# Performance work log

Measured on AMD Instinct MI355X. Metric: run time of the kernel, lower is better.

The kernel has to match this reference:

```python
import jax, jax.numpy as jnp
import numpy as np

HIDDEN_DIM = 128


def setup_inputs() -> dict:
    key = jax.random.key(0)
    ks = jax.random.split(key, 7)
    n_edges, edge_dim, edge_hidden, d = 20000, 16, 128, HIDDEN_DIM
    h_v = jax.random.normal(ks[0], (n_edges, d), dtype=jnp.float32)
    h_w = jax.random.normal(ks[1], (n_edges, d), dtype=jnp.float32)
    edge_features = jax.random.normal(ks[2], (n_edges, edge_dim), dtype=jnp.float32)
    W1 = jax.random.normal(ks[3], (edge_dim, edge_hidden), dtype=jnp.float32) * (1.0 / np.sqrt(edge_dim))
    b1 = jnp.zeros((edge_hidden,), dtype=jnp.float32)
    W2 = jax.random.normal(ks[4], (edge_hidden, d * d), dtype=jnp.float32) * (1.0 / np.sqrt(edge_hidden))
    b2 = jnp.zeros((d * d,), dtype=jnp.float32)
    return {"h_v": h_v, "h_w": h_w, "edge_features": edge_features,
            "W1": W1, "b1": b1, "W2": W2, "b2": b2}


def reference(h_v, h_w, edge_features, W1, b1, W2, b2):
    d = HIDDEN_DIM
    # Edge MLP: edge_dim -> edge_hidden -> d*d
    hidden = jax.nn.relu(edge_features @ W1 + b1)          # (E, edge_hidden)
    A = (hidden @ W2 + b2).reshape(-1, d, d)               # (E, d, d) per-edge matrices
    # Batched matrix-vector product: messages_e = A_e @ h_w_e
    messages = jnp.einsum('eij,ej->ei', A, h_w)            # (E, d)
    return messages
```

## Files before the change

### kernel.cpp

```cpp
#include <hip/hip_runtime.h>

#define E_EDGES 20000
#define D_DIM   128
#define HS      136

#define NBA 136
#define NBH 313
#define NBC 320

#define SLAB_B 21504

typedef _Float16 f16x8 __attribute__((ext_vector_type(8)));
typedef _Float16 f16x2 __attribute__((ext_vector_type(2)));
typedef float    floatx4 __attribute__((ext_vector_type(4)));

union F8 { f16x8 v; f16x2 h2[4]; unsigned int u[4]; };

__device__ __forceinline__ unsigned short f32_to_f16(float f) {
    _Float16 h = (_Float16)f;
    return __builtin_bit_cast(unsigned short, h);
}

__device__ __forceinline__ void gload_lds16(const void* g, void* l) {
    __builtin_amdgcn_global_load_lds(
        (const __attribute__((address_space(1))) unsigned int*)g,
        (__attribute__((address_space(3))) unsigned int*)l, 16, 0, 0);
}

__global__ __launch_bounds__(256) void prep_all(
    const float* __restrict__ W2, const float* __restrict__ b2,
    const float* __restrict__ ef, const float* __restrict__ W1,
    const float* __restrict__ b1, const float* __restrict__ hw,
    uint4* __restrict__ bpf, char* __restrict__ hslab,
    unsigned short* __restrict__ hwb)
{
    __shared__ __align__(16) char pmem[34816];
    const int bx = blockIdx.x;
    const int t  = threadIdx.x;

    if (bx < NBA) {
        const int h = bx;
        if (h < 129) {
            unsigned short* tile = (unsigned short*)pmem;
            const float* src = (h < 128) ? (W2 + (size_t)h * (D_DIM * D_DIM)) : b2;
            #pragma unroll
            for (int r = 0; r < 16; ++r) {
                const float4 v = ((const float4*)src)[r * 256 + t];
                int c   = (r * 256 + t) * 4;
                int col = c >> 7;
                int k   = c & 127;
                unsigned int u0 = f32_to_f16(v.x) | ((unsigned int)f32_to_f16(v.y) << 16);
                unsigned int u1 = f32_to_f16(v.z) | ((unsigned int)f32_to_f16(v.w) << 16);
                *(uint2*)&tile[col * 136 + k] = make_uint2(u0, u1);
            }
            __syncthreads();
            #pragma unroll
            for (int r2 = 0; r2 < 8; ++r2) {
                int cidx = r2 * 256 + t;
                int ll = cidx & 63;
                int nt = (cidx >> 6) & 1;
                int jq = (cidx >> 7) & 3;
                int ch = (cidx >> 9) & 3;
                int col = 32 * ch + 16 * nt + (ll & 15);
                int k0  = 32 * jq + 8 * (ll >> 4);
                bpf[(size_t)h * 2048 + cidx] = *(const uint4*)&tile[col * 136 + k0];
            }
        } else {
            #pragma unroll
            for (int r2 = 0; r2 < 8; ++r2)
                bpf[(size_t)h * 2048 + r2 * 256 + t] = make_uint4(0, 0, 0, 0);
        }
    } else if (bx < NBA + NBH) {
        float* W1s = (float*)pmem;
        float* b1s = (float*)(pmem + 8192);
        float (*efs)[17] = (float(*)[17])(pmem + 8704);
        const int b  = bx - NBA;
        const int e0 = b * 64;
        #pragma unroll
        for (int i = 0; i < 2; ++i)
            *(float4*)&W1s[(i * 256 + t) * 4] = ((const float4*)W1)[i * 256 + t];
        if (t < 32) *(float4*)&b1s[t * 4] = ((const float4*)b1)[t];
        {
            int e  = t >> 2;
            int k4 = (t & 3) * 4;
            int ge = e0 + e;
            float4 v = make_float4(0.f, 0.f, 0.f, 0.f);
            if (ge < E_EDGES) v = *(const float4*)(ef + (size_t)ge * 16 + k4);
            efs[e][k4 + 0] = v.x; efs[e][k4 + 1] = v.y;
            efs[e][k4 + 2] = v.z; efs[e][k4 + 3] = v.w;
        }
        __syncthreads();
        const int e  = t & 63;
        const int hg = t >> 6;
        const int ge = e0 + e;
        const bool valid = ge < E_EDGES;
        const int eg = ge / 80;
        const int re = ge - eg * 80;
        char* slab = hslab + (size_t)eg * SLAB_B + re * 264;
        float efr[16];
        #pragma unroll
        for (int k = 0; k < 16; ++k) efr[k] = efs[e][k];
        #pragma unroll 4
        for (int hi2 = 0; hi2 < 16; ++hi2) {
            const int h0 = hg * 32 + 2 * hi2;
            float2 bb = *(const float2*)&b1s[h0];
            float a0 = bb.x, a1 = bb.y;
            #pragma unroll
            for (int k = 0; k < 16; ++k) {
                float2 wv = *(const float2*)&W1s[k * 128 + h0];
                a0 += efr[k] * wv.x;
                a1 += efr[k] * wv.y;
            }
            unsigned int pk = (unsigned int)f32_to_f16(fmaxf(a0, 0.f))
                            | ((unsigned int)f32_to_f16(fmaxf(a1, 0.f)) << 16);
            if (valid) *(unsigned int*)(slab + h0 * 2) = pk;
        }
        if (hg == 0 && valid) {
            *(unsigned int*)(slab + 128 * 2) = 0x00003C00u;
            *(unsigned int*)(slab + 130 * 2) = 0u;
        }
    } else {
        int i0 = (bx - NBA - NBH) * 256 + t;
        for (int i = i0; i < (E_EDGES * D_DIM) / 4; i += NBC * 256) {
            const float4 v = ((const float4*)hw)[i];
            union { unsigned short u16[4]; uint2 u2; } o;
            o.u16[0] = f32_to_f16(v.x);
            o.u16[1] = f32_to_f16(v.y);
            o.u16[2] = f32_to_f16(v.z);
            o.u16[3] = f32_to_f16(v.w);
            ((uint2*)hwb)[i] = o.u2;
        }
    }
}

__global__ __launch_bounds__(256, 4)
void edge_main(const uint4* __restrict__ bpf, const char* __restrict__ hslab,
               const uint4* __restrict__ hwb, float* __restrict__ out) {
    __shared__ __align__(16) char slab[SLAB_B];
    const int bx  = blockIdx.x;
    const int ch  = (bx & 7) >> 1;
    const int eg  = (bx >> 3) * 2 + (bx & 1);
    const int tid = threadIdx.x;
    const int jq  = tid >> 6;
    const int l   = tid & 63;
    const int l4  = l >> 4;
    const int lm  = l & 15;
    const int e0  = eg * 80;

    {
        const char* src = hslab + (size_t)eg * SLAB_B;
        for (int i = jq; i < 21; i += 4)
            gload_lds16(src + i * 1024 + l * 16, slab + i * 1024);
    }

    F8 hws[5];
    #pragma unroll
    for (int m = 0; m < 5; ++m)
        hws[m].v = ((const F8*)hwb)[(e0 + 16 * m + lm) * 16 + 4 * jq + l4].v;

    floatx4 C[5][2];
    #pragma unroll
    for (int m = 0; m < 5; ++m)
        #pragma unroll
        for (int nt = 0; nt < 2; ++nt)
            C[m][nt] = (floatx4){0.f, 0.f, 0.f, 0.f};

    __syncthreads();

    const f16x8* bpf8 = (const f16x8*)bpf;
    const int cbase = ch * 512 + jq * 128 + l;

    f16x8 B[2][2];
    auto loadB = [&](int h, f16x8 (&Bq)[2]) {
        const f16x8* p = bpf8 + (size_t)h * 2048 + cbase;
        Bq[0] = p[0];
        Bq[1] = p[64];
    };
    auto doH = [&](int h, const uint2 (&hid)[5]) {
        const int hh = h & 3, p = h & 1;
        #pragma unroll
        for (int m = 0; m < 5; ++m) {
            unsigned int s   = (hh < 2) ? hid[m].x : hid[m].y;
            unsigned int sel = (hh & 1) ? 0x03020302u : 0x01000100u;
            f16x2 d = __builtin_bit_cast(f16x2, __builtin_amdgcn_perm(0u, s, sel));
            F8 a;
            #pragma unroll
            for (int i = 0; i < 4; ++i) a.h2[i] = hws[m].h2[i] * d;
            C[m][0] = __builtin_amdgcn_mfma_f32_16x16x32_f16(a.v, B[p][0], C[m][0], 0, 0, 0);
            C[m][1] = __builtin_amdgcn_mfma_f32_16x16x32_f16(a.v, B[p][1], C[m][1], 0, 0, 0);
        }
        loadB(h + 2, B[p]);
    };

    loadB(0, B[0]);
    loadB(1, B[1]);
    for (int q = 0; q < 33; ++q) {
        uint2 hid[5];
        #pragma unroll
        for (int m = 0; m < 5; ++m)
            hid[m] = *(const uint2*)(slab + (16 * m + lm) * 264 + q * 8);
        doH(4 * q + 0, hid);
        doH(4 * q + 1, hid);
        doH(4 * q + 2, hid);
        doH(4 * q + 3, hid);
    }

    float* red = (float*)slab;
    #pragma unroll 1
    for (int src = 1; src < 4; ++src) {
        __syncthreads();
        if (jq == src) {
            #pragma unroll
            for (int m = 0; m < 5; ++m)
                #pragma unroll
                for (int nt = 0; nt < 2; ++nt)
                    #pragma unroll
                    for (int r = 0; r < 4; ++r)
                        red[((m * 2 + nt) * 4 + r) * 64 + l] = C[m][nt][r];
        }
        __syncthreads();
        if (jq == 0) {
            #pragma unroll
            for (int m = 0; m < 5; ++m)
                #pragma unroll
                for (int nt = 0; nt < 2; ++nt)
                    #pragma unroll
                    for (int r = 0; r < 4; ++r)
                        C[m][nt][r] += red[((m * 2 + nt) * 4 + r) * 64 + l];
        }
    }
    if (jq == 0) {
        #pragma unroll
        for (int m = 0; m < 5; ++m)
            #pragma unroll
            for (int nt = 0; nt < 2; ++nt)
                #pragma unroll
                for (int r = 0; r < 4; ++r)
                    out[(size_t)(e0 + 16 * m + 4 * l4 + r) * D_DIM
                        + 32 * ch + 16 * nt + lm] = C[m][nt][r];
    }
}

extern "C" void kernel_launch(void* const* d_in, const int* in_sizes, int n_in,
                              void* d_out, int out_size, void* d_ws, size_t ws_size,
                              hipStream_t stream) {
    const float* h_w = (const float*)d_in[1];
    const float* ef  = (const float*)d_in[2];
    const float* W1  = (const float*)d_in[3];
    const float* b1  = (const float*)d_in[4];
    const float* W2  = (const float*)d_in[5];
    const float* b2  = (const float*)d_in[6];
    float* out = (float*)d_out;

    char* ws = (char*)d_ws;
    uint4*          bpf   = (uint4*)ws;
    char*           hslab = ws + 4456448;
    unsigned short* hwb   = (unsigned short*)(ws + 4456448 + 5376000);

    hipLaunchKernelGGL(prep_all, dim3(NBA + NBH + NBC), dim3(256), 0, stream,
                       W2, b2, ef, W1, b1, h_w, bpf, hslab, hwb);
    hipLaunchKernelGGL(edge_main, dim3(1000), dim3(256), 0, stream,
                       bpf, hslab, (const uint4*)hwb, out);
}
```

Baseline: 163.6 us.

## Fuse edge MLP hidden layer and h_w conversion into main kernel, widen column tile

The first-layer edge MLP is now computed inside the main kernel with a small fp16 MFMA per 80-edge group and written straight to LDS. h_w is converted to fp16 in registers. This removes the hidden slab and fp16 h_w staging buffers and their extra global round trip. Each block now covers 64 output columns instead of 32, so there are 500 blocks instead of 1000. That halves redundant hidden-layer and h_w work per edge group, but it doubles accumulator registers and lowers the occupancy target to 2 blocks per SIMD group.

New measurement: 161.2 us. About the same (-1.5%).

```diff
diff --git a/kernel.cpp b/kernel.cpp
--- a/kernel.cpp
+++ b/kernel.cpp
@@ -2,144 +2,70 @@
 
 #define E_EDGES 20000
 #define D_DIM   128
-#define HS      136
-
-#define NBA 136
-#define NBH 313
-#define NBC 320
-
-#define SLAB_B 21504
+#define NBA     136
+#define SLAB_B  21504
 
 typedef _Float16 f16x8 __attribute__((ext_vector_type(8)));
+typedef _Float16 f16x4 __attribute__((ext_vector_type(4)));
 typedef _Float16 f16x2 __attribute__((ext_vector_type(2)));
 typedef float    floatx4 __attribute__((ext_vector_type(4)));
 
 union F8 { f16x8 v; f16x2 h2[4]; unsigned int u[4]; };
+union F4 { f16x4 v; f16x2 h2[2]; unsigned int u[2]; };
 
 __device__ __forceinline__ unsigned short f32_to_f16(float f) {
     _Float16 h = (_Float16)f;
     return __builtin_bit_cast(unsigned short, h);
 }
 
-__device__ __forceinline__ void gload_lds16(const void* g, void* l) {
-    __builtin_amdgcn_global_load_lds(
-        (const __attribute__((address_space(1))) unsigned int*)g,
-        (__attribute__((address_space(3))) unsigned int*)l, 16, 0, 0);
-}
-
-__global__ __launch_bounds__(256) void prep_all(
+__global__ __launch_bounds__(256) void prep_w2(
     const float* __restrict__ W2, const float* __restrict__ b2,
-    const float* __restrict__ ef, const float* __restrict__ W1,
-    const float* __restrict__ b1, const float* __restrict__ hw,
-    uint4* __restrict__ bpf, char* __restrict__ hslab,
-    unsigned short* __restrict__ hwb)
+    uint4* __restrict__ bpf)
 {
-    __shared__ __align__(16) char pmem[34816];
-    const int bx = blockIdx.x;
-    const int t  = threadIdx.x;
-
-    if (bx < NBA) {
-        const int h = bx;
-        if (h < 129) {
-            unsigned short* tile = (unsigned short*)pmem;
-            const float* src = (h < 128) ? (W2 + (size_t)h * (D_DIM * D_DIM)) : b2;
-            #pragma unroll
-            for (int r = 0; r < 16; ++r) {
-                const float4 v = ((const float4*)src)[r * 256 + t];
-                int c   = (r * 256 + t) * 4;
-                int col = c >> 7;
-                int k   = c & 127;
-                unsigned int u0 = f32_to_f16(v.x) | ((unsigned int)f32_to_f16(v.y) << 16);
-                unsigned int u1 = f32_to_f16(v.z) | ((unsigned int)f32_to_f16(v.w) << 16);
-                *(uint2*)&tile[col * 136 + k] = make_uint2(u0, u1);
-            }
-            __syncthreads();
-            #pragma unroll
-            for (int r2 = 0; r2 < 8; ++r2) {
-                int cidx = r2 * 256 + t;
-                int ll = cidx & 63;
-                int nt = (cidx >> 6) & 1;
-                int jq = (cidx >> 7) & 3;
-                int ch = (cidx >> 9) & 3;
-                int col = 32 * ch + 16 * nt + (ll & 15);
-                int k0  = 32 * jq + 8 * (ll >> 4);
-                bpf[(size_t)h * 2048 + cidx] = *(const uint4*)&tile[col * 136 + k0];
-            }
-        } else {
-            #pragma unroll
-            for (int r2 = 0; r2 < 8; ++r2)
-                bpf[(size_t)h * 2048 + r2 * 256 + t] = make_uint4(0, 0, 0, 0);
-        }
-    } else if (bx < NBA + NBH) {
-        float* W1s = (float*)pmem;
-        float* b1s = (float*)(pmem + 8192);
-        float (*efs)[17] = (float(*)[17])(pmem + 8704);
-        const int b  = bx - NBA;
-        const int e0 = b * 64;
-        #pragma unroll
-        for (int i = 0; i < 2; ++i)
-            *(float4*)&W1s[(i * 256 + t) * 4] = ((const float4*)W1)[i * 256 + t];
-        if (t < 32) *(float4*)&b1s[t * 4] = ((const float4*)b1)[t];
-        {
-            int e  = t >> 2;
-            int k4 = (t & 3) * 4;
-            int ge = e0 + e;
-            float4 v = make_float4(0.f, 0.f, 0.f, 0.f);
-            if (ge < E_EDGES) v = *(const float4*)(ef + (size_t)ge * 16 + k4);
-            efs[e][k4 + 0] = v.x; efs[e][k4 + 1] = v.y;
-            efs[e][k4 + 2] = v.z; efs[e][k4 + 3] = v.w;
+    __shared__ __align__(16) unsigned short tile[17408];
+    const int h = blockIdx.x;
+    const int t = threadIdx.x;
+
+    if (h < 129) {
+        const float* src = (h < 128) ? (W2 + (size_t)h * (D_DIM * D_DIM)) : b2;
+        #pragma unroll
+        for (int r = 0; r < 16; ++r) {
+            const float4 v = ((const float4*)src)[r * 256 + t];
+            int c   = (r * 256 + t) * 4;
+            int col = c >> 7;
+            int k   = c & 127;
+            unsigned int u0 = f32_to_f16(v.x) | ((unsigned int)f32_to_f16(v.y) << 16);
+            unsigned int u1 = f32_to_f16(v.z) | ((unsigned int)f32_to_f16(v.w) << 16);
+            *(uint2*)&tile[col * 136 + k] = make_uint2(u0, u1);
         }
         __syncthreads();
-        const int e  = t & 63;
-        const int hg = t >> 6;
-        const int ge = e0 + e;
-        const bool valid = ge < E_EDGES;
-        const int eg = ge / 80;
-        const int re = ge - eg * 80;
-        char* slab = hslab + (size_t)eg * SLAB_B + re * 264;
-        float efr[16];
-        #pragma unroll
-        for (int k = 0; k < 16; ++k) efr[k] = efs[e][k];
-        #pragma unroll 4
-        for (int hi2 = 0; hi2 < 16; ++hi2) {
-            const int h0 = hg * 32 + 2 * hi2;
-            float2 bb = *(const float2*)&b1s[h0];
-            float a0 = bb.x, a1 = bb.y;
-            #pragma unroll
-            for (int k = 0; k < 16; ++k) {
-                float2 wv = *(const float2*)&W1s[k * 128 + h0];
-                a0 += efr[k] * wv.x;
-                a1 += efr[k] * wv.y;
-            }
-            unsigned int pk = (unsigned int)f32_to_f16(fmaxf(a0, 0.f))
-                            | ((unsigned int)f32_to_f16(fmaxf(a1, 0.f)) << 16);
-            if (valid) *(unsigned int*)(slab + h0 * 2) = pk;
-        }
-        if (hg == 0 && valid) {
-            *(unsigned int*)(slab + 128 * 2) = 0x00003C00u;
-            *(unsigned int*)(slab + 130 * 2) = 0u;
+        #pragma unroll
+        for (int r2 = 0; r2 < 8; ++r2) {
+            int cidx = r2 * 256 + t;
+            int ll = cidx & 63;
+            int nt = (cidx >> 6) & 1;
+            int jq = (cidx >> 7) & 3;
+            int ch = (cidx >> 9) & 3;
+            int col = 32 * ch + 16 * nt + (ll & 15);
+            int k0  = 32 * jq + 8 * (ll >> 4);
+            bpf[(size_t)h * 2048 + cidx] = *(const uint4*)&tile[col * 136 + k0];
         }
     } else {
-        int i0 = (bx - NBA - NBH) * 256 + t;
-        for (int i = i0; i < (E_EDGES * D_DIM) / 4; i += NBC * 256) {
-            const float4 v = ((const float4*)hw)[i];
-            union { unsigned short u16[4]; uint2 u2; } o;
-            o.u16[0] = f32_to_f16(v.x);
-            o.u16[1] = f32_to_f16(v.y);
-            o.u16[2] = f32_to_f16(v.z);
-            o.u16[3] = f32_to_f16(v.w);
-            ((uint2*)hwb)[i] = o.u2;
-        }
-    }
-}
-
-__global__ __launch_bounds__(256, 4)
-void edge_main(const uint4* __restrict__ bpf, const char* __restrict__ hslab,
-               const uint4* __restrict__ hwb, float* __restrict__ out) {
+        #pragma unroll
+        for (int r2 = 0; r2 < 8; ++r2)
+            bpf[(size_t)h * 2048 + r2 * 256 + t] = make_uint4(0, 0, 0, 0);
+    }
+}
+
+__global__ __launch_bounds__(256, 2)
+void edge_main(const uint4* __restrict__ bpf, const float* __restrict__ hw,
+               const float* __restrict__ ef, const float* __restrict__ W1,
+               const float* __restrict__ b1, float* __restrict__ out)
+{
     __shared__ __align__(16) char slab[SLAB_B];
     const int bx  = blockIdx.x;
-    const int ch  = (bx & 7) >> 1;
-    const int eg  = (bx >> 3) * 2 + (bx & 1);
+    const int ch2 = bx & 1;
+    const int eg  = bx >> 1;
     const int tid = threadIdx.x;
     const int jq  = tid >> 6;
     const int l   = tid & 63;
@@ -148,36 +74,81 @@
     const int e0  = eg * 80;
 
     {
-        const char* src = hslab + (size_t)eg * SLAB_B;
-        for (int i = jq; i < 21; i += 4)
-            gload_lds16(src + i * 1024 + l * 16, slab + i * 1024);
+        F4 A[5];
+        #pragma unroll
+        for (int m = 0; m < 5; ++m) {
+            const float4 q4 = *(const float4*)(ef + (size_t)(e0 + 16 * m + lm) * 16 + 4 * l4);
+            A[m].h2[0] = (f16x2){(_Float16)q4.x, (_Float16)q4.y};
+            A[m].h2[1] = (f16x2){(_Float16)q4.z, (_Float16)q4.w};
+        }
+        F4 Bw[2];
+        float bv[2];
+        #pragma unroll
+        for (int nn = 0; nn < 2; ++nn) {
+            const int col = jq * 32 + nn * 16 + lm;
+            float w0 = W1[(4 * l4 + 0) * 128 + col];
+            float w1 = W1[(4 * l4 + 1) * 128 + col];
+            float w2 = W1[(4 * l4 + 2) * 128 + col];
+            float w3 = W1[(4 * l4 + 3) * 128 + col];
+            Bw[nn].h2[0] = (f16x2){(_Float16)w0, (_Float16)w1};
+            Bw[nn].h2[1] = (f16x2){(_Float16)w2, (_Float16)w3};
+            bv[nn] = b1[col];
+        }
+        #pragma unroll
+        for (int m = 0; m < 5; ++m) {
+            floatx4 H0 = (floatx4){bv[0], bv[0], bv[0], bv[0]};
+            floatx4 H1 = (floatx4){bv[1], bv[1], bv[1], bv[1]};
+            H0 = __builtin_amdgcn_mfma_f32_16x16x16f16(A[m].v, Bw[0].v, H0, 0, 0, 0);
+            H1 = __builtin_amdgcn_mfma_f32_16x16x16f16(A[m].v, Bw[1].v, H1, 0, 0, 0);
+            #pragma unroll
+            for (int r = 0; r < 4; ++r) {
+                const int e = 16 * m + 4 * l4 + r;
+                *(unsigned short*)(slab + e * 264 + (jq * 32 + lm) * 2) =
+                    f32_to_f16(fmaxf(H0[r], 0.f));
+                *(unsigned short*)(slab + e * 264 + (jq * 32 + 16 + lm) * 2) =
+                    f32_to_f16(fmaxf(H1[r], 0.f));
+            }
+        }
+        if (tid < 80) {
+            *(unsigned int*)(slab + tid * 264 + 256) = 0x00003C00u;
+            *(unsigned int*)(slab + tid * 264 + 260) = 0u;
+        }
     }
 
     F8 hws[5];
     #pragma unroll
-    for (int m = 0; m < 5; ++m)
-        hws[m].v = ((const F8*)hwb)[(e0 + 16 * m + lm) * 16 + 4 * jq + l4].v;
-
-    floatx4 C[5][2];
+    for (int m = 0; m < 5; ++m) {
+        const float* ph = hw + (size_t)(e0 + 16 * m + lm) * 128 + 32 * jq + 8 * l4;
+        const float4 x = *(const float4*)ph;
+        const float4 y = *(const float4*)(ph + 4);
+        hws[m].h2[0] = (f16x2){(_Float16)x.x, (_Float16)x.y};
+        hws[m].h2[1] = (f16x2){(_Float16)x.z, (_Float16)x.w};
+        hws[m].h2[2] = (f16x2){(_Float16)y.x, (_Float16)y.y};
+        hws[m].h2[3] = (f16x2){(_Float16)y.z, (_Float16)y.w};
+    }
+
+    floatx4 C[5][4];
     #pragma unroll
     for (int m = 0; m < 5; ++m)
         #pragma unroll
-        for (int nt = 0; nt < 2; ++nt)
-            C[m][nt] = (floatx4){0.f, 0.f, 0.f, 0.f};
+        for (int ct = 0; ct < 4; ++ct)
+            C[m][ct] = (floatx4){0.f, 0.f, 0.f, 0.f};
 
     __syncthreads();
 
     const f16x8* bpf8 = (const f16x8*)bpf;
-    const int cbase = ch * 512 + jq * 128 + l;
-
-    f16x8 B[2][2];
-    auto loadB = [&](int h, f16x8 (&Bq)[2]) {
+    const int cbase = ch2 * 1024 + jq * 128 + l;
+
+    f16x8 B[2][4];
+    auto loadB = [&](int h, f16x8 (&Bq)[4]) {
         const f16x8* p = bpf8 + (size_t)h * 2048 + cbase;
         Bq[0] = p[0];
         Bq[1] = p[64];
+        Bq[2] = p[512];
+        Bq[3] = p[576];
     };
     auto doH = [&](int h, const uint2 (&hid)[5]) {
-        const int hh = h & 3, p = h & 1;
+        const int hh = h & 3, pp = h & 1;
         #pragma unroll
         for (int m = 0; m < 5; ++m) {
             unsigned int s   = (hh < 2) ? hid[m].x : hid[m].y;
@@ -186,10 +157,12 @@
             F8 a;
             #pragma unroll
             for (int i = 0; i < 4; ++i) a.h2[i] = hws[m].h2[i] * d;
-            C[m][0] = __builtin_amdgcn_mfma_f32_16x16x32_f16(a.v, B[p][0], C[m][0], 0, 0, 0);
-            C[m][1] = __builtin_amdgcn_mfma_f32_16x16x32_f16(a.v, B[p][1], C[m][1], 0, 0, 0);
-        }
-        loadB(h + 2, B[p]);
+            C[m][0] = __builtin_amdgcn_mfma_f32_16x16x32_f16(a.v, B[pp][0], C[m][0], 0, 0, 0);
+            C[m][1] = __builtin_amdgcn_mfma_f32_16x16x32_f16(a.v, B[pp][1], C[m][1], 0, 0, 0);
+            C[m][2] = __builtin_amdgcn_mfma_f32_16x16x32_f16(a.v, B[pp][2], C[m][2], 0, 0, 0);
+            C[m][3] = __builtin_amdgcn_mfma_f32_16x16x32_f16(a.v, B[pp][3], C[m][3], 0, 0, 0);
+        }
+        loadB(h + 2, B[pp]);
     };
 
     loadB(0, B[0]);
@@ -213,31 +186,31 @@
             #pragma unroll
             for (int m = 0; m < 5; ++m)
                 #pragma unroll
-                for (int nt = 0; nt < 2; ++nt)
+                for (int ct = 0; ct < 4; ++ct)
                     #pragma unroll
                     for (int r = 0; r < 4; ++r)
-                        red[((m * 2 + nt) * 4 + r) * 64 + l] = C[m][nt][r];
+                        red[((m * 4 + ct) * 4 + r) * 64 + l] = C[m][ct][r];
         }
         __syncthreads();
         if (jq == 0) {
             #pragma unroll
             for (int m = 0; m < 5; ++m)
                 #pragma unroll
-                for (int nt = 0; nt < 2; ++nt)
+                for (int ct = 0; ct < 4; ++ct)
                     #pragma unroll
                     for (int r = 0; r < 4; ++r)
-                        C[m][nt][r] += red[((m * 2 + nt) * 4 + r) * 64 + l];
+                        C[m][ct][r] += red[((m * 4 + ct) * 4 + r) * 64 + l];
         }
     }
     if (jq == 0) {
         #pragma unroll
         for (int m = 0; m < 5; ++m)
             #pragma unroll
-            for (int nt = 0; nt < 2; ++nt)
+            for (int ct = 0; ct < 4; ++ct)
                 #pragma unroll
                 for (int r = 0; r < 4; ++r)
                     out[(size_t)(e0 + 16 * m + 4 * l4 + r) * D_DIM
-                        + 32 * ch + 16 * nt + lm] = C[m][nt][r];
+                        + 64 * ch2 + 16 * ct + lm] = C[m][ct][r];
     }
 }
 
@@ -252,13 +225,9 @@
     const float* b2  = (const float*)d_in[6];
     float* out = (float*)d_out;
 
-    char* ws = (char*)d_ws;
-    uint4*          bpf   = (uint4*)ws;
-    char*           hslab = ws + 4456448;
-    unsigned short* hwb   = (unsigned short*)(ws + 4456448 + 5376000);
-
-    hipLaunchKernelGGL(prep_all, dim3(NBA + NBH + NBC), dim3(256), 0, stream,
-                       W2, b2, ef, W1, b1, h_w, bpf, hslab, hwb);
-    hipLaunchKernelGGL(edge_main, dim3(1000), dim3(256), 0, stream,
-                       bpf, hslab, (const uint4*)hwb, out);
-}
+    uint4* bpf = (uint4*)d_ws;
+
+    hipLaunchKernelGGL(prep_w2, dim3(NBA), dim3(256), 0, stream, W2, b2, bpf);
+    hipLaunchKernelGGL(edge_main, dim3(500), dim3(256), 0, stream,
+                       bpf, h_w, ef, W1, b1, out);
+}
```
